# Kernel optimization log

Hardware: AMD Instinct MI355X
Metric: run time of the kernel (lower is better)

## Reference

```python
import jax, jax.numpy as jnp
import numpy as np

N = 50000      # nodes
E = 800000     # edges (avg degree 16)
D = 64         # input_dim
L = 64         # latent_dim


def setup_inputs() -> dict:
    key = jax.random.key(0)
    k1, k2, k3, k4, k5, k6 = jax.random.split(key, 6)
    x = jax.random.normal(k1, (N, D), dtype=jnp.float32)
    weight = jax.random.normal(k2, (D, L), dtype=jnp.float32) / np.sqrt(D)
    bias = jax.random.normal(k3, (L,), dtype=jnp.float32) * 0.01
    # strictly positive degrees to keep division well-behaved
    node_degree = jax.random.uniform(k4, (N, 1), dtype=jnp.float32) + 1.0
    edge_src = jax.random.randint(k5, (E,), 0, N, dtype=jnp.int32)
    edge_dst = jax.random.randint(k6, (E,), 0, N, dtype=jnp.int32)
    return {"x": x, "weight": weight, "bias": bias,
            "node_degree": node_degree,
            "edge_src": edge_src, "edge_dst": edge_dst}


def reference(x, weight, bias, node_degree, edge_src, edge_dst):
    # gnn_spmm(adj, x): sparse aggregate over incoming edges -> [N, D]
    agg = jax.ops.segment_sum(x[edge_src], edge_dst, num_segments=N)
    pooled = agg + x                      # residual self-connection
    node_linear = pooled @ weight + bias  # dense projection [N, L]
    normalized = node_linear / node_degree  # normalize_embedding == 2
    return jax.nn.relu(normalized)
```

## Files before the change

### kernel.cpp

```cpp
#include <hip/hip_runtime.h>
#include <hip/hip_fp16.h>

#define N_NODES 50000
#define DIM 64
#define CB 391
#define BNODES 128
#define CAP 2560
#define EPT 4
#define PLW 68

typedef _Float16 half8 __attribute__((ext_vector_type(8)));
typedef _Float16 half4v __attribute__((ext_vector_type(4)));
typedef float floatx4 __attribute__((ext_vector_type(4)));

#define WS_CURSOR  0
#define WS_COARSE  2048
#define WS_XH      (WS_COARSE + 4003840)
#define WS_WT      (WS_XH + 6400000)

__global__ void __launch_bounds__(256) convert_kernel(
        const float* __restrict__ x, const float* __restrict__ W,
        _Float16* __restrict__ xh, _Float16* __restrict__ wt,
        int* __restrict__ bucket_cursor) {
    int b = blockIdx.x, t = threadIdx.x;
    if (b < 3125) {
        int i = b * 256 + t;
        float4 v = reinterpret_cast<const float4*>(x)[i];
        half4v h = { (_Float16)v.x, (_Float16)v.y, (_Float16)v.z, (_Float16)v.w };
        reinterpret_cast<half4v*>(xh)[i] = h;
    } else {
        for (int i = t; i < CB; i += 256) bucket_cursor[i] = 0;
        #pragma unroll
        for (int i = 0; i < 16; ++i) {
            int idx = t * 16 + i;
            int n = idx >> 6, k = idx & 63;
            wt[idx] = (_Float16)W[k * DIM + n];
        }
    }
}

__global__ void __launch_bounds__(256) partition_kernel(
        const int* __restrict__ edge_src,
        const int* __restrict__ edge_dst,
        int* __restrict__ bucket_cursor,
        unsigned int* __restrict__ coarse,
        int E) {
    __shared__ int lhist[CB];
    __shared__ int lbase[CB];
    int t = threadIdx.x;
    for (int i = t; i < CB; i += 256) lhist[i] = 0;
    __syncthreads();

    int base_e = blockIdx.x * (256 * EPT);
    unsigned int pk[EPT];
    int bk[EPT];
    #pragma unroll
    for (int j = 0; j < EPT; ++j) {
        int e = base_e + j * 256 + t;
        bk[j] = -1;
        if (e < E) {
            int s = edge_src[e];
            int d = edge_dst[e];
            bk[j] = d >> 7;
            pk[j] = ((unsigned int)s << 7) | (unsigned int)(d & 127);
            atomicAdd(&lhist[bk[j]], 1);
        }
    }
    __syncthreads();

    for (int i = t; i < CB; i += 256) {
        lbase[i] = atomicAdd(&bucket_cursor[i], lhist[i]);
        lhist[i] = 0;
    }
    __syncthreads();

    #pragma unroll
    for (int j = 0; j < EPT; ++j) {
        if (bk[j] >= 0) {
            int r = atomicAdd(&lhist[bk[j]], 1);
            coarse[(size_t)bk[j] * CAP + lbase[bk[j]] + r] = pk[j];
        }
    }
}

__global__ void __launch_bounds__(512) fused_kernel(
        const float* __restrict__ x,
        const _Float16* __restrict__ xh,
        const _Float16* __restrict__ wt,
        const float* __restrict__ bias,
        const float* __restrict__ deg,
        const int* __restrict__ bucket_cursor,
        const unsigned int* __restrict__ coarse,
        float* __restrict__ out) {
    __shared__ unsigned int sedges[CAP];
    __shared__ float pl[BNODES * PLW];
    __shared__ int hist[BNODES];
    __shared__ int excl[BNODES];
    __shared__ int cur[BNODES];

    int t = threadIdx.x;
    int b = blockIdx.x;
    int nb = b * BNODES;
    int cnt = bucket_cursor[b];
    const unsigned int* cbk = coarse + (size_t)b * CAP;

    if (t < BNODES) hist[t] = 0;
    __syncthreads();
    for (int i = t; i < cnt; i += 512) {
        atomicAdd(&hist[cbk[i] & 127u], 1);
    }
    __syncthreads();

    if (t < BNODES) excl[t] = hist[t];
    __syncthreads();
    #pragma unroll
    for (int off = 1; off < BNODES; off <<= 1) {
        int u = 0;
        if (t < BNODES && t >= off) u = excl[t - off];
        __syncthreads();
        if (t < BNODES) excl[t] += u;
        __syncthreads();
    }
    if (t < BNODES) {
        int ex = excl[t] - hist[t];
        excl[t] = ex;
        cur[t]  = ex;
    }
    __syncthreads();

    for (int i = t; i < cnt; i += 512) {
        unsigned int e = cbk[i];
        int p = atomicAdd(&cur[e & 127u], 1);
        sedges[p] = e >> 7;
    }
    __syncthreads();

    int g = t >> 3;
    int c = t & 7;
    #pragma unroll
    for (int pass = 0; pass < 2; ++pass) {
        int loc = g + pass * 64;
        int node = nb + loc;
        float acc[8];
        #pragma unroll
        for (int j = 0; j < 8; ++j) acc[j] = 0.f;
        int off = excl[loc];
        int ct = (node < N_NODES) ? hist[loc] : 0;
        for (int k = 0; k < ct; ++k) {
            int src = (int)sedges[off + k];
            half8 v = *reinterpret_cast<const half8*>(
                xh + (size_t)src * DIM + c * 8);
            #pragma unroll
            for (int j = 0; j < 8; ++j) acc[j] += (float)v[j];
        }
        if (node < N_NODES) {
            const float4 r0 = *reinterpret_cast<const float4*>(
                x + (size_t)node * DIM + c * 8);
            const float4 r1 = *reinterpret_cast<const float4*>(
                x + (size_t)node * DIM + c * 8 + 4);
            float* p = &pl[loc * PLW + c * 8];
            p[0] = acc[0] + r0.x; p[1] = acc[1] + r0.y;
            p[2] = acc[2] + r0.z; p[3] = acc[3] + r0.w;
            p[4] = acc[4] + r1.x; p[5] = acc[5] + r1.y;
            p[6] = acc[6] + r1.z; p[7] = acc[7] + r1.w;
        }
    }
    __syncthreads();

    int wv = t >> 6;
    int lane = t & 63;
    int m = lane & 15;
    int q = lane >> 4;
    int lbase = wv * 16;

    const float* ap = &pl[(lbase + m) * PLW];
    half8 a0, a1;
    #pragma unroll
    for (int j = 0; j < 8; ++j) a0[j] = (_Float16)ap[q * 8 + j];
    #pragma unroll
    for (int j = 0; j < 8; ++j) a1[j] = (_Float16)ap[32 + q * 8 + j];

    floatx4 acc4[4];
    #pragma unroll
    for (int tt = 0; tt < 4; ++tt) {
        half8 b0 = *reinterpret_cast<const half8*>(wt + (size_t)(tt * 16 + m) * DIM + q * 8);
        half8 b1 = *reinterpret_cast<const half8*>(wt + (size_t)(tt * 16 + m) * DIM + q * 8 + 32);
        floatx4 cfrag = {0.f, 0.f, 0.f, 0.f};
        cfrag = __builtin_amdgcn_mfma_f32_16x16x32_f16(a0, b0, cfrag, 0, 0, 0);
        cfrag = __builtin_amdgcn_mfma_f32_16x16x32_f16(a1, b1, cfrag, 0, 0, 0);
        acc4[tt] = cfrag;
    }

    #pragma unroll
    for (int r = 0; r < 4; ++r) {
        int row = q * 4 + r;
        int node = nb + lbase + row;
        if (node < N_NODES) {
            float inv = 1.0f / deg[node];
            #pragma unroll
            for (int tt = 0; tt < 4; ++tt) {
                float v = (acc4[tt][r] + bias[tt * 16 + m]) * inv;
                out[(size_t)node * DIM + tt * 16 + m] = fmaxf(v, 0.f);
            }
        }
    }
}

extern "C" void kernel_launch(void* const* d_in, const int* in_sizes, int n_in,
                              void* d_out, int out_size, void* d_ws, size_t ws_size,
                              hipStream_t stream) {
    const float* x        = (const float*)d_in[0];
    const float* weight   = (const float*)d_in[1];
    const float* bias     = (const float*)d_in[2];
    const float* node_deg = (const float*)d_in[3];
    const int*   edge_src = (const int*)d_in[4];
    const int*   edge_dst = (const int*)d_in[5];
    float* out = (float*)d_out;
    const int E = in_sizes[4];

    char* ws = (char*)d_ws;
    int*          bucket_cursor = (int*)(ws + WS_CURSOR);
    unsigned int* coarse        = (unsigned int*)(ws + WS_COARSE);
    _Float16*     xh            = (_Float16*)(ws + WS_XH);
    _Float16*     wt            = (_Float16*)(ws + WS_WT);

    convert_kernel<<<3126, 256, 0, stream>>>(x, weight, xh, wt, bucket_cursor);

    int pa_blocks = (E + 256 * EPT - 1) / (256 * EPT);
    partition_kernel<<<pa_blocks, 256, 0, stream>>>(
        edge_src, edge_dst, bucket_cursor, coarse, E);

    fused_kernel<<<CB, 512, 0, stream>>>(
        x, xh, wt, bias, node_deg, bucket_cursor, coarse, out);
}
```

Measured before the change: 124.9 us.

## Merge partition into prep kernel, split fused blocks in half, unroll gather

Moves edge partitioning into the conversion kernel with larger per-block edge chunks (6400 edges) and zeroes the cursor with a memset, removing one kernel launch. The fused kernel now runs two 256-thread blocks per 128-node bucket, each handling 64 nodes and filtering the bucket's edges, using a wave shuffle scan instead of the barrier-based scan. The gather loop is unrolled by 4 to issue more independent loads. Each bucket's edge list is now read twice, and the shared edge buffer (SCAP=1344) could overflow if a half-bucket gets more edges than that.

```diff
diff --git a/kernel.cpp b/kernel.cpp
--- a/kernel.cpp
+++ b/kernel.cpp
@@ -4,10 +4,10 @@
 #define N_NODES 50000
 #define DIM 64
 #define CB 391
-#define BNODES 128
 #define CAP 2560
-#define EPT 4
+#define EB 6400
 #define PLW 68
+#define SCAP 1344
 
 typedef _Float16 half8 __attribute__((ext_vector_type(8)));
 typedef _Float16 half4v __attribute__((ext_vector_type(4)));
@@ -18,18 +18,45 @@
 #define WS_XH      (WS_COARSE + 4003840)
 #define WS_WT      (WS_XH + 6400000)
 
-__global__ void __launch_bounds__(256) convert_kernel(
+__global__ void __launch_bounds__(256) prep_kernel(
         const float* __restrict__ x, const float* __restrict__ W,
+        const int* __restrict__ edge_src, const int* __restrict__ edge_dst,
         _Float16* __restrict__ xh, _Float16* __restrict__ wt,
-        int* __restrict__ bucket_cursor) {
+        int* __restrict__ bucket_cursor, unsigned int* __restrict__ coarse,
+        int E, int pa) {
     int b = blockIdx.x, t = threadIdx.x;
-    if (b < 3125) {
-        int i = b * 256 + t;
+    if (b < pa) {
+        __shared__ int lhist[CB];
+        __shared__ int lbase[CB];
+        for (int i = t; i < CB; i += 256) lhist[i] = 0;
+        __syncthreads();
+
+        int base = b * EB;
+        int end = base + EB; if (end > E) end = E;
+
+        for (int i = base + t; i < end; i += 256) {
+            atomicAdd(&lhist[edge_dst[i] >> 7], 1);
+        }
+        __syncthreads();
+        for (int i = t; i < CB; i += 256) {
+            lbase[i] = atomicAdd(&bucket_cursor[i], lhist[i]);
+            lhist[i] = 0;
+        }
+        __syncthreads();
+        for (int i = base + t; i < end; i += 256) {
+            int s = edge_src[i];
+            int d = edge_dst[i];
+            int bk = d >> 7;
+            int r = atomicAdd(&lhist[bk], 1);
+            coarse[(size_t)bk * CAP + lbase[bk] + r] =
+                ((unsigned int)s << 7) | (unsigned int)(d & 127);
+        }
+    } else if (b < pa + 3125) {
+        int i = (b - pa) * 256 + t;
         float4 v = reinterpret_cast<const float4*>(x)[i];
         half4v h = { (_Float16)v.x, (_Float16)v.y, (_Float16)v.z, (_Float16)v.w };
         reinterpret_cast<half4v*>(xh)[i] = h;
     } else {
-        for (int i = t; i < CB; i += 256) bucket_cursor[i] = 0;
         #pragma unroll
         for (int i = 0; i < 16; ++i) {
             int idx = t * 16 + i;
@@ -39,51 +66,7 @@
     }
 }
 
-__global__ void __launch_bounds__(256) partition_kernel(
-        const int* __restrict__ edge_src,
-        const int* __restrict__ edge_dst,
-        int* __restrict__ bucket_cursor,
-        unsigned int* __restrict__ coarse,
-        int E) {
-    __shared__ int lhist[CB];
-    __shared__ int lbase[CB];
-    int t = threadIdx.x;
-    for (int i = t; i < CB; i += 256) lhist[i] = 0;
-    __syncthreads();
-
-    int base_e = blockIdx.x * (256 * EPT);
-    unsigned int pk[EPT];
-    int bk[EPT];
-    #pragma unroll
-    for (int j = 0; j < EPT; ++j) {
-        int e = base_e + j * 256 + t;
-        bk[j] = -1;
-        if (e < E) {
-            int s = edge_src[e];
-            int d = edge_dst[e];
-            bk[j] = d >> 7;
-            pk[j] = ((unsigned int)s << 7) | (unsigned int)(d & 127);
-            atomicAdd(&lhist[bk[j]], 1);
-        }
-    }
-    __syncthreads();
-
-    for (int i = t; i < CB; i += 256) {
-        lbase[i] = atomicAdd(&bucket_cursor[i], lhist[i]);
-        lhist[i] = 0;
-    }
-    __syncthreads();
-
-    #pragma unroll
-    for (int j = 0; j < EPT; ++j) {
-        if (bk[j] >= 0) {
-            int r = atomicAdd(&lhist[bk[j]], 1);
-            coarse[(size_t)bk[j] * CAP + lbase[bk[j]] + r] = pk[j];
-        }
-    }
-}
-
-__global__ void __launch_bounds__(512) fused_kernel(
+__global__ void __launch_bounds__(256) fused_kernel(
         const float* __restrict__ x,
         const _Float16* __restrict__ xh,
         const _Float16* __restrict__ wt,
@@ -92,46 +75,49 @@
         const int* __restrict__ bucket_cursor,
         const unsigned int* __restrict__ coarse,
         float* __restrict__ out) {
-    __shared__ unsigned int sedges[CAP];
-    __shared__ float pl[BNODES * PLW];
-    __shared__ int hist[BNODES];
-    __shared__ int excl[BNODES];
-    __shared__ int cur[BNODES];
+    __shared__ unsigned int sedges[SCAP];
+    __shared__ float pl[64 * PLW];
+    __shared__ int hist[64];
+    __shared__ int excl[64];
+    __shared__ int cur[64];
 
     int t = threadIdx.x;
     int b = blockIdx.x;
-    int nb = b * BNODES;
-    int cnt = bucket_cursor[b];
-    const unsigned int* cbk = coarse + (size_t)b * CAP;
-
-    if (t < BNODES) hist[t] = 0;
-    __syncthreads();
-    for (int i = t; i < cnt; i += 512) {
-        atomicAdd(&hist[cbk[i] & 127u], 1);
-    }
-    __syncthreads();
-
-    if (t < BNODES) excl[t] = hist[t];
-    __syncthreads();
-    #pragma unroll
-    for (int off = 1; off < BNODES; off <<= 1) {
-        int u = 0;
-        if (t < BNODES && t >= off) u = excl[t - off];
-        __syncthreads();
-        if (t < BNODES) excl[t] += u;
-        __syncthreads();
-    }
-    if (t < BNODES) {
-        int ex = excl[t] - hist[t];
-        excl[t] = ex;
-        cur[t]  = ex;
-    }
-    __syncthreads();
-
-    for (int i = t; i < cnt; i += 512) {
+    int bucket = b >> 1;
+    int half = b & 1;
+    int nb = b * 64;
+    int cnt = bucket_cursor[bucket];
+    const unsigned int* cbk = coarse + (size_t)bucket * CAP;
+
+    if (t < 64) hist[t] = 0;
+    __syncthreads();
+    for (int i = t; i < cnt; i += 256) {
         unsigned int e = cbk[i];
-        int p = atomicAdd(&cur[e & 127u], 1);
-        sedges[p] = e >> 7;
+        int loc = (int)(e & 127u);
+        if ((loc >> 6) == half) atomicAdd(&hist[loc & 63], 1);
+    }
+    __syncthreads();
+
+    if (t < 64) {
+        int v = hist[t];
+        int s = v;
+        #pragma unroll
+        for (int off = 1; off < 64; off <<= 1) {
+            int u = __shfl_up(s, off);
+            if (t >= off) s += u;
+        }
+        excl[t] = s - v;
+        cur[t]  = s - v;
+    }
+    __syncthreads();
+
+    for (int i = t; i < cnt; i += 256) {
+        unsigned int e = cbk[i];
+        int loc = (int)(e & 127u);
+        if ((loc >> 6) == half) {
+            int p = atomicAdd(&cur[loc & 63], 1);
+            sedges[p] = e >> 7;
+        }
     }
     __syncthreads();
 
@@ -139,19 +125,34 @@
     int c = t & 7;
     #pragma unroll
     for (int pass = 0; pass < 2; ++pass) {
-        int loc = g + pass * 64;
+        int loc = g + pass * 32;
         int node = nb + loc;
         float acc[8];
         #pragma unroll
         for (int j = 0; j < 8; ++j) acc[j] = 0.f;
         int off = excl[loc];
         int ct = (node < N_NODES) ? hist[loc] : 0;
-        for (int k = 0; k < ct; ++k) {
-            int src = (int)sedges[off + k];
-            half8 v = *reinterpret_cast<const half8*>(
-                xh + (size_t)src * DIM + c * 8);
+        int k = 0;
+        for (; k + 4 <= ct; k += 4) {
+            int s0 = (int)sedges[off + k + 0];
+            int s1 = (int)sedges[off + k + 1];
+            int s2 = (int)sedges[off + k + 2];
+            int s3 = (int)sedges[off + k + 3];
+            half8 v0 = *reinterpret_cast<const half8*>(xh + (size_t)s0 * DIM + c * 8);
+            half8 v1 = *reinterpret_cast<const half8*>(xh + (size_t)s1 * DIM + c * 8);
+            half8 v2 = *reinterpret_cast<const half8*>(xh + (size_t)s2 * DIM + c * 8);
+            half8 v3 = *reinterpret_cast<const half8*>(xh + (size_t)s3 * DIM + c * 8);
             #pragma unroll
-            for (int j = 0; j < 8; ++j) acc[j] += (float)v[j];
+            for (int j = 0; j < 8; ++j) {
+                acc[j] += (float)v0[j]; acc[j] += (float)v1[j];
+                acc[j] += (float)v2[j]; acc[j] += (float)v3[j];
+            }
+        }
+        for (; k < ct; ++k) {
+            int s0 = (int)sedges[off + k];
+            half8 v0 = *reinterpret_cast<const half8*>(xh + (size_t)s0 * DIM + c * 8);
+            #pragma unroll
+            for (int j = 0; j < 8; ++j) acc[j] += (float)v0[j];
         }
         if (node < N_NODES) {
             const float4 r0 = *reinterpret_cast<const float4*>(
@@ -224,12 +225,12 @@
     _Float16*     xh            = (_Float16*)(ws + WS_XH);
     _Float16*     wt            = (_Float16*)(ws + WS_WT);
 
-    convert_kernel<<<3126, 256, 0, stream>>>(x, weight, xh, wt, bucket_cursor);
-
-    int pa_blocks = (E + 256 * EPT - 1) / (256 * EPT);
-    partition_kernel<<<pa_blocks, 256, 0, stream>>>(
-        edge_src, edge_dst, bucket_cursor, coarse, E);
-
-    fused_kernel<<<CB, 512, 0, stream>>>(
+    hipMemsetAsync(bucket_cursor, 0, CB * sizeof(int), stream);
+
+    int pa = (E + EB - 1) / EB;
+    prep_kernel<<<pa + 3125 + 1, 256, 0, stream>>>(
+        x, weight, edge_src, edge_dst, xh, wt, bucket_cursor, coarse, E, pa);
+
+    fused_kernel<<<2 * CB, 256, 0, stream>>>(
         x, xh, wt, bias, node_deg, bucket_cursor, coarse, out);
 }
```

New measurement: 120.1 us. -3.8%, faster.
